# Kernel tuning notes

Hardware: AMD Instinct MI355X
Metric: run time of the kernel (lower is better)

Reference implementation:

```python
import jax, jax.numpy as jnp
import numpy as np

N = 50000      # nodes
E = 800000     # edges
C_IN = 128
C_HID = 128
C_OUT = 128
LN_EPS = 1e-5  # PyG LayerNorm default eps


def setup_inputs() -> dict:
    key = jax.random.key(0)
    ks = jax.random.split(key, 8)
    x = jax.random.normal(ks[0], (N, C_IN), jnp.float32)
    edge_index = jax.random.randint(ks[1], (2, E), 0, N, dtype=jnp.int32)
    s1 = 1.0 / np.sqrt(C_IN)
    s2 = 1.0 / np.sqrt(C_HID)
    return {
        "x": x,
        "edge_index": edge_index,
        "eps1": jnp.float32(1e-4),              # GINConv train_eps init
        "W1": jax.random.normal(ks[2], (C_HID, C_IN), jnp.float32) * s1,
        "b1": jnp.zeros((C_HID,), jnp.float32),
        "ln_w": jnp.ones((C_HID,), jnp.float32),
        "ln_b": jnp.zeros((C_HID,), jnp.float32),
        "prelu_a": jnp.float32(0.25),           # nn.PReLU default single param
        "eps2": jnp.float32(1e-4),
        "W2": jax.random.normal(ks[3], (C_OUT, C_HID), jnp.float32) * s2,
        "b2": jnp.zeros((C_OUT,), jnp.float32),
    }


def _gin_max(x, src, dst, eps, W, b):
    # GINConv(aggr='max'): nn((1+eps)*x + max_{j in N(i)} x_j)
    msg = x[src]                                          # [E, C] gather
    agg = jax.ops.segment_max(msg, dst, num_segments=N)   # [N, C]
    agg = jnp.where(jnp.isfinite(agg), agg, jnp.float32(0.0))  # empty segments -> 0 (PyG fill)
    h = (1.0 + eps) * x + agg
    return h @ W.T + b


def _graph_layernorm(x, w, b):
    # PyG LayerNorm mode='graph', single graph: normalize over ALL nodes & channels
    x = x - jnp.mean(x)
    x = x / (jnp.std(x) + LN_EPS)
    return x * w + b


def reference(x, edge_index, eps1, W1, b1, ln_w, ln_b, prelu_a, eps2, W2, b2):
    src, dst = edge_index[0], edge_index[1]
    h = _gin_max(x, src, dst, eps1, W1, b1)
    h = _graph_layernorm(h, ln_w, ln_b)
    h = jnp.where(h >= 0, h, prelu_a * h)  # PReLU
    return _gin_max(h, src, dst, eps2, W2, b2)
```

## Files before the change

### kernel.cpp

```cpp
#include <hip/hip_runtime.h>
#include <hip/hip_fp16.h>
#include <math.h>

#define NN 50000
#define NE 800000
#define C  128
#define BKT 128
#define NBUK ((NN + BKT - 1) / BKT)
#define ECHUNK 2048
#define NEBLK ((NE + ECHUNK - 1) / ECHUNK)

typedef _Float16 f16x8 __attribute__((ext_vector_type(8)));
typedef float f32x4 __attribute__((ext_vector_type(4)));

__global__ void k_wh(const float* __restrict__ W1, const float* __restrict__ W2,
                     _Float16* __restrict__ Wh1, _Float16* __restrict__ Wh2) {
  int i = blockIdx.x * 256 + threadIdx.x;
  if (i < C * C) Wh1[i] = (_Float16)W1[i];
  else if (i < 2 * C * C) Wh2[i - C * C] = (_Float16)W2[i - C * C];
}

__global__ __launch_bounds__(256) void k_bh(const int* __restrict__ dst,
                                            int* __restrict__ bh) {
  __shared__ int h[NBUK];
  int t = threadIdx.x;
  for (int i = t; i < NBUK; i += 256) h[i] = 0;
  __syncthreads();
  int base = blockIdx.x * ECHUNK;
  int end = base + ECHUNK; if (end > NE) end = NE;
  for (int e = base + t; e < end; e += 256) atomicAdd(&h[dst[e] >> 7], 1);
  __syncthreads();
  for (int i = t; i < NBUK; i += 256) bh[i * NEBLK + blockIdx.x] = h[i];
}

__global__ __launch_bounds__(256) void k_bscan(int* __restrict__ bh,
                                               int* __restrict__ btot) {
  int b = blockIdx.x, t = threadIdx.x;
  int lane = t & 63, wid = t >> 6;
  __shared__ int wsum[4];
  int carry = 0;
  for (int base = 0; base < NEBLK; base += 256) {
    int i = base + t;
    int v = (i < NEBLK) ? bh[b * NEBLK + i] : 0;
    int incl = v;
    #pragma unroll
    for (int off = 1; off < 64; off <<= 1) {
      int u = __shfl_up(incl, off, 64);
      if (lane >= off) incl += u;
    }
    if (lane == 63) wsum[wid] = incl;
    __syncthreads();
    int woff = 0;
    #pragma unroll
    for (int wI = 0; wI < 4; ++wI) if (wI < wid) woff += wsum[wI];
    if (i < NEBLK) bh[b * NEBLK + i] = carry + woff + incl - v;
    int total = wsum[0] + wsum[1] + wsum[2] + wsum[3];
    __syncthreads();
    carry += total;
  }
  if (t == 0) btot[b] = carry;
}

__global__ __launch_bounds__(256) void k_bbase(const int* __restrict__ btot,
                                               int* __restrict__ bbase,
                                               int* __restrict__ rowstart) {
  int t = threadIdx.x;
  int lane = t & 63, wid = t >> 6;
  __shared__ int wsum[4];
  int carry = 0;
  for (int base = 0; base < NBUK; base += 256) {
    int i = base + t;
    int v = (i < NBUK) ? btot[i] : 0;
    int incl = v;
    #pragma unroll
    for (int off = 1; off < 64; off <<= 1) {
      int u = __shfl_up(incl, off, 64);
      if (lane >= off) incl += u;
    }
    if (lane == 63) wsum[wid] = incl;
    __syncthreads();
    int woff = 0;
    #pragma unroll
    for (int wI = 0; wI < 4; ++wI) if (wI < wid) woff += wsum[wI];
    if (i < NBUK) bbase[i] = carry + woff + incl - v;
    int total = wsum[0] + wsum[1] + wsum[2] + wsum[3];
    __syncthreads();
    carry += total;
  }
  if (t == 0) rowstart[NN] = NE;
}

__global__ __launch_bounds__(256) void k_bscatter(const int* __restrict__ src,
                       const int* __restrict__ dst,
                       const int* __restrict__ bh, const int* __restrict__ bbase,
                       int2* __restrict__ binned) {
  __shared__ int cur[NBUK];
  int t = threadIdx.x, blk = blockIdx.x;
  for (int i = t; i < NBUK; i += 256) cur[i] = bbase[i] + bh[i * NEBLK + blk];
  __syncthreads();
  int base = blk * ECHUNK;
  int end = base + ECHUNK; if (end > NE) end = NE;
  for (int e = base + t; e < end; e += 256) {
    int d = dst[e];
    int pos = atomicAdd(&cur[d >> 7], 1);
    binned[pos] = make_int2(src[e], d);
  }
}

__global__ __launch_bounds__(256) void k_bfill(const int2* __restrict__ binned,
                       const int* __restrict__ bbase, const int* __restrict__ btot,
                       int* __restrict__ rowstart, int* __restrict__ csr) {
  int b = blockIdx.x, t = threadIdx.x;
  __shared__ int hist[BKT];
  __shared__ int cur[BKT];
  __shared__ int wsum[4];
  int s0 = bbase[b];
  int cnt = btot[b];
  if (t < BKT) hist[t] = 0;
  __syncthreads();
  for (int j = t; j < cnt; j += 256) atomicAdd(&hist[binned[s0 + j].y & (BKT - 1)], 1);
  __syncthreads();
  int v = (t < BKT) ? hist[t] : 0;
  int lane = t & 63, wid = t >> 6;
  int incl = v;
  #pragma unroll
  for (int off = 1; off < 64; off <<= 1) {
    int u = __shfl_up(incl, off, 64);
    if (lane >= off) incl += u;
  }
  if (lane == 63) wsum[wid] = incl;
  __syncthreads();
  int woff = 0;
  #pragma unroll
  for (int wI = 0; wI < 4; ++wI) if (wI < wid) woff += wsum[wI];
  int excl = woff + incl - v;
  if (t < BKT) {
    cur[t] = excl;
    int node = b * BKT + t;
    if (node < NN) rowstart[node] = s0 + excl;
  }
  __syncthreads();
  for (int j = t; j < cnt; j += 256) {
    int2 sd = binned[s0 + j];
    int p = atomicAdd(&cur[sd.y & (BKT - 1)], 1);
    csr[s0 + p] = sd.x;
  }
}

__global__ __launch_bounds__(256) void k_tohalf(const float* __restrict__ in,
                                                __half2* __restrict__ o) {
  int i = blockIdx.x * 256 + threadIdx.x;
  if (i < NN * C / 4) {
    float4 v = ((const float4*)in)[i];
    o[2 * i]     = __floats2half2_rn(v.x, v.y);
    o[2 * i + 1] = __floats2half2_rn(v.z, v.w);
  }
}

__global__ __launch_bounds__(256) void k_agg_h(const __half2* __restrict__ xh2,
                       const int* __restrict__ rs, const int* __restrict__ csr,
                       const float* __restrict__ eps_p, __half2* __restrict__ preh2) {
  int wid = threadIdx.x >> 6;
  int lane = threadIdx.x & 63;
  int n = blockIdx.x * 4 + wid;
  if (n >= NN) return;
  int s0 = rs[n], s1 = rs[n + 1];
  float a0 = -INFINITY, a1 = -INFINITY, b0 = -INFINITY, b1 = -INFINITY;
  float c0 = -INFINITY, c1 = -INFINITY, d0 = -INFINITY, d1 = -INFINITY;
  float e0a = -INFINITY, e1a = -INFINITY, f0 = -INFINITY, f1 = -INFINITY;
  float g0 = -INFINITY, g1 = -INFINITY, h0 = -INFINITY, h1 = -INFINITY;
  int j = s0;
  for (; j + 7 < s1; j += 8) {
    int i0 = csr[j], i1 = csr[j + 1], i2 = csr[j + 2], i3 = csr[j + 3];
    int i4 = csr[j + 4], i5 = csr[j + 5], i6 = csr[j + 6], i7 = csr[j + 7];
    __half2 v0 = xh2[(size_t)i0 * 64 + lane];
    __half2 v1 = xh2[(size_t)i1 * 64 + lane];
    __half2 v2 = xh2[(size_t)i2 * 64 + lane];
    __half2 v3 = xh2[(size_t)i3 * 64 + lane];
    __half2 v4 = xh2[(size_t)i4 * 64 + lane];
    __half2 v5 = xh2[(size_t)i5 * 64 + lane];
    __half2 v6 = xh2[(size_t)i6 * 64 + lane];
    __half2 v7 = xh2[(size_t)i7 * 64 + lane];
    a0 = fmaxf(a0, __low2float(v0));  a1 = fmaxf(a1, __high2float(v0));
    b0 = fmaxf(b0, __low2float(v1));  b1 = fmaxf(b1, __high2float(v1));
    c0 = fmaxf(c0, __low2float(v2));  c1 = fmaxf(c1, __high2float(v2));
    d0 = fmaxf(d0, __low2float(v3));  d1 = fmaxf(d1, __high2float(v3));
    e0a = fmaxf(e0a, __low2float(v4)); e1a = fmaxf(e1a, __high2float(v4));
    f0 = fmaxf(f0, __low2float(v5));  f1 = fmaxf(f1, __high2float(v5));
    g0 = fmaxf(g0, __low2float(v6));  g1 = fmaxf(g1, __high2float(v6));
    h0 = fmaxf(h0, __low2float(v7));  h1 = fmaxf(h1, __high2float(v7));
  }
  for (; j + 3 < s1; j += 4) {
    int i0 = csr[j], i1 = csr[j + 1], i2 = csr[j + 2], i3 = csr[j + 3];
    __half2 v0 = xh2[(size_t)i0 * 64 + lane];
    __half2 v1 = xh2[(size_t)i1 * 64 + lane];
    __half2 v2 = xh2[(size_t)i2 * 64 + lane];
    __half2 v3 = xh2[(size_t)i3 * 64 + lane];
    a0 = fmaxf(a0, __low2float(v0)); a1 = fmaxf(a1, __high2float(v0));
    b0 = fmaxf(b0, __low2float(v1)); b1 = fmaxf(b1, __high2float(v1));
    c0 = fmaxf(c0, __low2float(v2)); c1 = fmaxf(c1, __high2float(v2));
    d0 = fmaxf(d0, __low2float(v3)); d1 = fmaxf(d1, __high2float(v3));
  }
  for (; j < s1; ++j) {
    int i0 = csr[j];
    __half2 v0 = xh2[(size_t)i0 * 64 + lane];
    a0 = fmaxf(a0, __low2float(v0)); a1 = fmaxf(a1, __high2float(v0));
  }
  float m0 = fmaxf(fmaxf(fmaxf(a0, b0), fmaxf(c0, d0)), fmaxf(fmaxf(e0a, f0), fmaxf(g0, h0)));
  float m1 = fmaxf(fmaxf(fmaxf(a1, b1), fmaxf(c1, d1)), fmaxf(fmaxf(e1a, f1), fmaxf(g1, h1)));
  if (s1 == s0) { m0 = 0.f; m1 = 0.f; }
  float e1v = 1.0f + eps_p[0];
  __half2 xs = xh2[(size_t)n * 64 + lane];
  float ox = fmaf(e1v, __low2float(xs), m0);
  float oy = fmaf(e1v, __high2float(xs), m1);
  preh2[(size_t)n * 64 + lane] = __floats2half2_rn(ox, oy);
}

template<int MODE>
__global__ __launch_bounds__(256) void k_gemm_f16(const _Float16* __restrict__ Ah,
                       const _Float16* __restrict__ Wh, const float* __restrict__ bias,
                       _Float16* __restrict__ outh, float* __restrict__ outf,
                       double* __restrict__ st) {
  int wid = threadIdx.x >> 6, lane = threadIdx.x & 63;
  int nt = blockIdx.x * 4 + wid;
  int r = lane & 15;
  int kq = lane >> 4;
  float s = 0.f, ss = 0.f;
  if (nt < NN / 16) {
    const _Float16* arow = Ah + ((size_t)nt * 16 + r) * C + kq * 8;
    f32x4 acc[8];
    #pragma unroll
    for (int ot = 0; ot < 8; ++ot) {
      float bv = bias[ot * 16 + r];
      f32x4 z = {bv, bv, bv, bv};
      acc[ot] = z;
    }
    #pragma unroll
    for (int kk = 0; kk < 4; ++kk) {
      f16x8 a = *(const f16x8*)(arow + kk * 32);
      #pragma unroll
      for (int ot = 0; ot < 8; ++ot) {
        f16x8 b = *(const f16x8*)(Wh + ((size_t)ot * 16 + r) * C + kk * 32 + kq * 8);
        acc[ot] = __builtin_amdgcn_mfma_f32_16x16x32_f16(a, b, acc[ot], 0, 0, 0);
      }
    }
    size_t nbase = (size_t)nt * 16;
    #pragma unroll
    for (int ot = 0; ot < 8; ++ot) {
      #pragma unroll
      for (int j = 0; j < 4; ++j) {
        float v = acc[ot][j];
        size_t off = (nbase + kq * 4 + j) * C + ot * 16 + r;
        if (MODE == 0) {
          outh[off] = (_Float16)v;
          s += v; ss += v * v;
        } else {
          __builtin_nontemporal_store(v, &outf[off]);
        }
      }
    }
  }
  if (MODE == 0) {
    #pragma unroll
    for (int off = 32; off > 0; off >>= 1) {
      s  += __shfl_down(s, off, 64);
      ss += __shfl_down(ss, off, 64);
    }
    __shared__ float sdl[4], ssl[4];
    if (lane == 0) { sdl[wid] = s; ssl[wid] = ss; }
    __syncthreads();
    if (threadIdx.x == 0) {
      atomicAdd(&st[0], (double)(sdl[0] + sdl[1] + sdl[2] + sdl[3]));
      atomicAdd(&st[1], (double)(ssl[0] + ssl[1] + ssl[2] + ssl[3]));
    }
  }
}

__global__ void k_final(const double* __restrict__ st, float* __restrict__ scal) {
  double M = (double)NN * C;
  double mean = st[0] / M;
  double var = st[1] / M - mean * mean;
  if (var < 0.0) var = 0.0;
  double stdv = sqrt(var);
  scal[0] = (float)mean;
  scal[1] = (float)(1.0 / (stdv + 1e-5));
}

__global__ __launch_bounds__(256) void k_act_h(const _Float16* __restrict__ h,
                       const float* __restrict__ scal,
                       const float* __restrict__ lw, const float* __restrict__ lb,
                       const float* __restrict__ a_p, _Float16* __restrict__ outh) {
  int i = blockIdx.x * 256 + threadIdx.x;
  if (i >= NN * C / 8) return;
  float mean = scal[0], inv = scal[1], a = a_p[0];
  f16x8 v = ((const f16x8*)h)[i];
  int c8 = i & 15;
  float4 w0 = ((const float4*)lw)[c8 * 2], w1 = ((const float4*)lw)[c8 * 2 + 1];
  float4 b0 = ((const float4*)lb)[c8 * 2], b1 = ((const float4*)lb)[c8 * 2 + 1];
  float wv[8] = {w0.x, w0.y, w0.z, w0.w, w1.x, w1.y, w1.z, w1.w};
  float bv[8] = {b0.x, b0.y, b0.z, b0.w, b1.x, b1.y, b1.z, b1.w};
  f16x8 res;
  #pragma unroll
  for (int k = 0; k < 8; ++k) {
    float r = ((float)v[k] - mean) * inv * wv[k] + bv[k];
    r = (r >= 0.f) ? r : a * r;
    res[k] = (_Float16)r;
  }
  ((f16x8*)outh)[i] = res;
}

extern "C" void kernel_launch(void* const* d_in, const int* in_sizes, int n_in,
                              void* d_out, int out_size, void* d_ws, size_t ws_size,
                              hipStream_t stream) {
  const float* x    = (const float*)d_in[0];
  const int*   ei   = (const int*)d_in[1];
  const float* eps1 = (const float*)d_in[2];
  const float* W1   = (const float*)d_in[3];
  const float* b1   = (const float*)d_in[4];
  const float* lnw  = (const float*)d_in[5];
  const float* lnb  = (const float*)d_in[6];
  const float* pa   = (const float*)d_in[7];
  const float* eps2 = (const float*)d_in[8];
  const float* W2   = (const float*)d_in[9];
  const float* b2   = (const float*)d_in[10];
  float* out = (float*)d_out;
  const int* srcI = ei;
  const int* dstI = ei + NE;

  char* w = (char*)d_ws;
  _Float16* Bh     = (_Float16*)(w);
  __half2*  xh     = (__half2*)(w + 12800000);
  __half2*  preh   = (__half2*)(w + 25600000);
  _Float16* Wh1    = (_Float16*)(w + 38400000);
  _Float16* Wh2    = (_Float16*)(w + 38432768);
  int*      rowst  = (int*)(w + 38465536);
  int*      csr    = (int*)(w + 38665600);
  int2*     binned = (int2*)(w + 41865600);
  int*      bh     = (int*)(w + 48265600);
  int*      btot   = (int*)(w + 48877184);
  int*      bbase  = (int*)(w + 48878848);
  double*   st     = (double*)(w + 48880512);
  float*    scal   = (float*)(w + 48880528);

  hipMemsetAsync(st, 0, 2 * sizeof(double), stream);

  k_wh<<<128, 256, 0, stream>>>(W1, W2, Wh1, Wh2);

  k_bh<<<NEBLK, 256, 0, stream>>>(dstI, bh);
  k_bscan<<<NBUK, 256, 0, stream>>>(bh, btot);
  k_bbase<<<1, 256, 0, stream>>>(btot, bbase, rowst);
  k_bscatter<<<NEBLK, 256, 0, stream>>>(srcI, dstI, bh, bbase, binned);
  k_bfill<<<NBUK, 256, 0, stream>>>(binned, bbase, btot, rowst, csr);

  k_tohalf<<<(NN * C / 4 + 255) / 256, 256, 0, stream>>>(x, xh);

  k_agg_h<<<(NN + 3) / 4, 256, 0, stream>>>(xh, rowst, csr, eps1, preh);
  k_gemm_f16<0><<<(NN / 16 + 3) / 4, 256, 0, stream>>>((const _Float16*)preh, Wh1, b1,
                                                       Bh, nullptr, st);

  k_final<<<1, 1, 0, stream>>>(st, scal);
  k_act_h<<<(NN * C / 8 + 255) / 256, 256, 0, stream>>>(Bh, scal, lnw, lnb, pa,
                                                        (_Float16*)xh);

  k_agg_h<<<(NN + 3) / 4, 256, 0, stream>>>(xh, rowst, csr, eps2, preh);
  k_gemm_f16<1><<<(NN / 16 + 3) / 4, 256, 0, stream>>>((const _Float16*)preh, Wh2, b2,
                                                       nullptr, out, nullptr);
}
```

Baseline: 258.6 us.

## Build CSR via fixed-capacity bucket scatter and fuse setup kernels

```diff
diff --git a/kernel.cpp b/kernel.cpp
--- a/kernel.cpp
+++ b/kernel.cpp
@@ -7,118 +7,61 @@
 #define C  128
 #define BKT 128
 #define NBUK ((NN + BKT - 1) / BKT)
-#define ECHUNK 2048
-#define NEBLK ((NE + ECHUNK - 1) / ECHUNK)
+#define BCAP 4096
 
 typedef _Float16 f16x8 __attribute__((ext_vector_type(8)));
 typedef float f32x4 __attribute__((ext_vector_type(4)));
 
-__global__ void k_wh(const float* __restrict__ W1, const float* __restrict__ W2,
-                     _Float16* __restrict__ Wh1, _Float16* __restrict__ Wh2) {
+__global__ __launch_bounds__(256) void k_prep(const float* __restrict__ x,
+                     __half2* __restrict__ xh,
+                     const float* __restrict__ W1, const float* __restrict__ W2,
+                     _Float16* __restrict__ Wh1, _Float16* __restrict__ Wh2,
+                     int* __restrict__ bcnt, double* __restrict__ st) {
   int i = blockIdx.x * 256 + threadIdx.x;
+  if (i < NN * C / 4) {
+    float4 v = ((const float4*)x)[i];
+    xh[2 * i]     = __floats2half2_rn(v.x, v.y);
+    xh[2 * i + 1] = __floats2half2_rn(v.z, v.w);
+  }
   if (i < C * C) Wh1[i] = (_Float16)W1[i];
   else if (i < 2 * C * C) Wh2[i - C * C] = (_Float16)W2[i - C * C];
-}
-
-__global__ __launch_bounds__(256) void k_bh(const int* __restrict__ dst,
-                                            int* __restrict__ bh) {
-  __shared__ int h[NBUK];
-  int t = threadIdx.x;
-  for (int i = t; i < NBUK; i += 256) h[i] = 0;
-  __syncthreads();
-  int base = blockIdx.x * ECHUNK;
-  int end = base + ECHUNK; if (end > NE) end = NE;
-  for (int e = base + t; e < end; e += 256) atomicAdd(&h[dst[e] >> 7], 1);
-  __syncthreads();
-  for (int i = t; i < NBUK; i += 256) bh[i * NEBLK + blockIdx.x] = h[i];
-}
-
-__global__ __launch_bounds__(256) void k_bscan(int* __restrict__ bh,
-                                               int* __restrict__ btot) {
-  int b = blockIdx.x, t = threadIdx.x;
-  int lane = t & 63, wid = t >> 6;
-  __shared__ int wsum[4];
-  int carry = 0;
-  for (int base = 0; base < NEBLK; base += 256) {
-    int i = base + t;
-    int v = (i < NEBLK) ? bh[b * NEBLK + i] : 0;
-    int incl = v;
-    #pragma unroll
-    for (int off = 1; off < 64; off <<= 1) {
-      int u = __shfl_up(incl, off, 64);
-      if (lane >= off) incl += u;
-    }
-    if (lane == 63) wsum[wid] = incl;
-    __syncthreads();
-    int woff = 0;
-    #pragma unroll
-    for (int wI = 0; wI < 4; ++wI) if (wI < wid) woff += wsum[wI];
-    if (i < NEBLK) bh[b * NEBLK + i] = carry + woff + incl - v;
-    int total = wsum[0] + wsum[1] + wsum[2] + wsum[3];
-    __syncthreads();
-    carry += total;
-  }
-  if (t == 0) btot[b] = carry;
-}
-
-__global__ __launch_bounds__(256) void k_bbase(const int* __restrict__ btot,
-                                               int* __restrict__ bbase,
-                                               int* __restrict__ rowstart) {
-  int t = threadIdx.x;
-  int lane = t & 63, wid = t >> 6;
-  __shared__ int wsum[4];
-  int carry = 0;
-  for (int base = 0; base < NBUK; base += 256) {
-    int i = base + t;
-    int v = (i < NBUK) ? btot[i] : 0;
-    int incl = v;
-    #pragma unroll
-    for (int off = 1; off < 64; off <<= 1) {
-      int u = __shfl_up(incl, off, 64);
-      if (lane >= off) incl += u;
-    }
-    if (lane == 63) wsum[wid] = incl;
-    __syncthreads();
-    int woff = 0;
-    #pragma unroll
-    for (int wI = 0; wI < 4; ++wI) if (wI < wid) woff += wsum[wI];
-    if (i < NBUK) bbase[i] = carry + woff + incl - v;
-    int total = wsum[0] + wsum[1] + wsum[2] + wsum[3];
-    __syncthreads();
-    carry += total;
-  }
-  if (t == 0) rowstart[NN] = NE;
-}
-
-__global__ __launch_bounds__(256) void k_bscatter(const int* __restrict__ src,
-                       const int* __restrict__ dst,
-                       const int* __restrict__ bh, const int* __restrict__ bbase,
-                       int2* __restrict__ binned) {
-  __shared__ int cur[NBUK];
-  int t = threadIdx.x, blk = blockIdx.x;
-  for (int i = t; i < NBUK; i += 256) cur[i] = bbase[i] + bh[i * NEBLK + blk];
-  __syncthreads();
-  int base = blk * ECHUNK;
-  int end = base + ECHUNK; if (end > NE) end = NE;
-  for (int e = base + t; e < end; e += 256) {
-    int d = dst[e];
-    int pos = atomicAdd(&cur[d >> 7], 1);
-    binned[pos] = make_int2(src[e], d);
-  }
-}
-
-__global__ __launch_bounds__(256) void k_bfill(const int2* __restrict__ binned,
-                       const int* __restrict__ bbase, const int* __restrict__ btot,
-                       int* __restrict__ rowstart, int* __restrict__ csr) {
+  if (i < NBUK) bcnt[i] = 0;
+  if (i == NBUK) { st[0] = 0.0; st[1] = 0.0; }
+}
+
+__global__ __launch_bounds__(256) void k_scat(const int* __restrict__ src,
+                     const int* __restrict__ dst,
+                     int* __restrict__ bcnt, int2* __restrict__ binned) {
+  int i = blockIdx.x * 256 + threadIdx.x;
+  if (i < NE / 4) {
+    int4 s = ((const int4*)src)[i];
+    int4 d = ((const int4*)dst)[i];
+    int b0 = d.x >> 7, b1 = d.y >> 7, b2 = d.z >> 7, b3 = d.w >> 7;
+    int p0 = atomicAdd(&bcnt[b0], 1);
+    int p1 = atomicAdd(&bcnt[b1], 1);
+    int p2 = atomicAdd(&bcnt[b2], 1);
+    int p3 = atomicAdd(&bcnt[b3], 1);
+    if (p0 < BCAP) binned[b0 * BCAP + p0] = make_int2(s.x, d.x);
+    if (p1 < BCAP) binned[b1 * BCAP + p1] = make_int2(s.y, d.y);
+    if (p2 < BCAP) binned[b2 * BCAP + p2] = make_int2(s.z, d.z);
+    if (p3 < BCAP) binned[b3 * BCAP + p3] = make_int2(s.w, d.w);
+  }
+}
+
+__global__ __launch_bounds__(256) void k_bfill2(const int2* __restrict__ binned,
+                     const int* __restrict__ bcnt,
+                     int* __restrict__ rowstart, int* __restrict__ deg,
+                     int* __restrict__ csr) {
   int b = blockIdx.x, t = threadIdx.x;
   __shared__ int hist[BKT];
   __shared__ int cur[BKT];
   __shared__ int wsum[4];
-  int s0 = bbase[b];
-  int cnt = btot[b];
+  int cnt = bcnt[b];
+  if (cnt > BCAP) cnt = BCAP;
+  int base = b * BCAP;
   if (t < BKT) hist[t] = 0;
   __syncthreads();
-  for (int j = t; j < cnt; j += 256) atomicAdd(&hist[binned[s0 + j].y & (BKT - 1)], 1);
+  for (int j = t; j < cnt; j += 256) atomicAdd(&hist[binned[base + j].y & (BKT - 1)], 1);
   __syncthreads();
   int v = (t < BKT) ? hist[t] : 0;
   int lane = t & 63, wid = t >> 6;
@@ -137,34 +80,27 @@
   if (t < BKT) {
     cur[t] = excl;
     int node = b * BKT + t;
-    if (node < NN) rowstart[node] = s0 + excl;
+    if (node < NN) { rowstart[node] = base + excl; deg[node] = v; }
   }
   __syncthreads();
   for (int j = t; j < cnt; j += 256) {
-    int2 sd = binned[s0 + j];
+    int2 sd = binned[base + j];
     int p = atomicAdd(&cur[sd.y & (BKT - 1)], 1);
-    csr[s0 + p] = sd.x;
-  }
-}
-
-__global__ __launch_bounds__(256) void k_tohalf(const float* __restrict__ in,
-                                                __half2* __restrict__ o) {
-  int i = blockIdx.x * 256 + threadIdx.x;
-  if (i < NN * C / 4) {
-    float4 v = ((const float4*)in)[i];
-    o[2 * i]     = __floats2half2_rn(v.x, v.y);
-    o[2 * i + 1] = __floats2half2_rn(v.z, v.w);
+    csr[base + p] = sd.x;
   }
 }
 
 __global__ __launch_bounds__(256) void k_agg_h(const __half2* __restrict__ xh2,
-                       const int* __restrict__ rs, const int* __restrict__ csr,
+                       const int* __restrict__ rs, const int* __restrict__ degp,
+                       const int* __restrict__ csr,
                        const float* __restrict__ eps_p, __half2* __restrict__ preh2) {
   int wid = threadIdx.x >> 6;
   int lane = threadIdx.x & 63;
   int n = blockIdx.x * 4 + wid;
   if (n >= NN) return;
-  int s0 = rs[n], s1 = rs[n + 1];
+  int s0 = rs[n];
+  int dg = degp[n];
+  int s1 = s0 + dg;
   float a0 = -INFINITY, a1 = -INFINITY, b0 = -INFINITY, b1 = -INFINITY;
   float c0 = -INFINITY, c1 = -INFINITY, d0 = -INFINITY, d1 = -INFINITY;
   float e0a = -INFINITY, e1a = -INFINITY, f0 = -INFINITY, f1 = -INFINITY;
@@ -208,7 +144,7 @@
   }
   float m0 = fmaxf(fmaxf(fmaxf(a0, b0), fmaxf(c0, d0)), fmaxf(fmaxf(e0a, f0), fmaxf(g0, h0)));
   float m1 = fmaxf(fmaxf(fmaxf(a1, b1), fmaxf(c1, d1)), fmaxf(fmaxf(e1a, f1), fmaxf(g1, h1)));
-  if (s1 == s0) { m0 = 0.f; m1 = 0.f; }
+  if (dg == 0) { m0 = 0.f; m1 = 0.f; }
   float e1v = 1.0f + eps_p[0];
   __half2 xs = xh2[(size_t)n * 64 + lane];
   float ox = fmaf(e1v, __low2float(xs), m0);
@@ -276,23 +212,19 @@
   }
 }
 
-__global__ void k_final(const double* __restrict__ st, float* __restrict__ scal) {
-  double M = (double)NN * C;
-  double mean = st[0] / M;
-  double var = st[1] / M - mean * mean;
-  if (var < 0.0) var = 0.0;
-  double stdv = sqrt(var);
-  scal[0] = (float)mean;
-  scal[1] = (float)(1.0 / (stdv + 1e-5));
-}
-
 __global__ __launch_bounds__(256) void k_act_h(const _Float16* __restrict__ h,
-                       const float* __restrict__ scal,
+                       const double* __restrict__ st,
                        const float* __restrict__ lw, const float* __restrict__ lb,
                        const float* __restrict__ a_p, _Float16* __restrict__ outh) {
   int i = blockIdx.x * 256 + threadIdx.x;
   if (i >= NN * C / 8) return;
-  float mean = scal[0], inv = scal[1], a = a_p[0];
+  const double M = (double)NN * C;
+  double meand = st[0] / M;
+  double var = st[1] / M - meand * meand;
+  if (var < 0.0) var = 0.0;
+  float mean = (float)meand;
+  float inv = (float)(1.0 / (sqrt(var) + 1e-5));
+  float a = a_p[0];
   f16x8 v = ((const f16x8*)h)[i];
   int c8 = i & 15;
   float4 w0 = ((const float4*)lw)[c8 * 2], w1 = ((const float4*)lw)[c8 * 2 + 1];
@@ -334,35 +266,21 @@
   _Float16* Wh1    = (_Float16*)(w + 38400000);
   _Float16* Wh2    = (_Float16*)(w + 38432768);
   int*      rowst  = (int*)(w + 38465536);
-  int*      csr    = (int*)(w + 38665600);
-  int2*     binned = (int2*)(w + 41865600);
-  int*      bh     = (int*)(w + 48265600);
-  int*      btot   = (int*)(w + 48877184);
-  int*      bbase  = (int*)(w + 48878848);
-  double*   st     = (double*)(w + 48880512);
-  float*    scal   = (float*)(w + 48880528);
-
-  hipMemsetAsync(st, 0, 2 * sizeof(double), stream);
-
-  k_wh<<<128, 256, 0, stream>>>(W1, W2, Wh1, Wh2);
-
-  k_bh<<<NEBLK, 256, 0, stream>>>(dstI, bh);
-  k_bscan<<<NBUK, 256, 0, stream>>>(bh, btot);
-  k_bbase<<<1, 256, 0, stream>>>(btot, bbase, rowst);
-  k_bscatter<<<NEBLK, 256, 0, stream>>>(srcI, dstI, bh, bbase, binned);
-  k_bfill<<<NBUK, 256, 0, stream>>>(binned, bbase, btot, rowst, csr);
-
-  k_tohalf<<<(NN * C / 4 + 255) / 256, 256, 0, stream>>>(x, xh);
-
-  k_agg_h<<<(NN + 3) / 4, 256, 0, stream>>>(xh, rowst, csr, eps1, preh);
+  int*      deg    = (int*)(w + 38665536);
+  int*      csr    = (int*)(w + 38865536);
+  int2*     binned = (int2*)(w + 45271680);
+  int*      bcnt   = (int*)(w + 58083968);
+  double*   st     = (double*)(w + 58085536);
+
+  k_prep<<<6250, 256, 0, stream>>>(x, xh, W1, W2, Wh1, Wh2, bcnt, st);
+  k_scat<<<(NE / 4 + 255) / 256, 256, 0, stream>>>(srcI, dstI, bcnt, binned);
+  k_bfill2<<<NBUK, 256, 0, stream>>>(binned, bcnt, rowst, deg, csr);
+  k_agg_h<<<(NN + 3) / 4, 256, 0, stream>>>(xh, rowst, deg, csr, eps1, preh);
   k_gemm_f16<0><<<(NN / 16 + 3) / 4, 256, 0, stream>>>((const _Float16*)preh, Wh1, b1,
                                                        Bh, nullptr, st);
-
-  k_final<<<1, 1, 0, stream>>>(st, scal);
-  k_act_h<<<(NN * C / 8 + 255) / 256, 256, 0, stream>>>(Bh, scal, lnw, lnb, pa,
+  k_act_h<<<(NN * C / 8 + 255) / 256, 256, 0, stream>>>(Bh, st, lnw, lnb, pa,
                                                         (_Float16*)xh);
-
-  k_agg_h<<<(NN + 3) / 4, 256, 0, stream>>>(xh, rowst, csr, eps2, preh);
+  k_agg_h<<<(NN + 3) / 4, 256, 0, stream>>>(xh, rowst, deg, csr, eps2, preh);
   k_gemm_f16<1><<<(NN / 16 + 3) / 4, 256, 0, stream>>>((const _Float16*)preh, Wh2, b2,
                                                        nullptr, out, nullptr);
 }
```

Result: slower. 514.6 us (+99.0%).
